# Kernel tuning notes

Hardware: AMD Instinct MI355X
Metric: run time of the kernel (lower is better)

The kernel has to match this reference:

```python
import jax, jax.numpy as jnp
import numpy as np


def _linear_interp(t, S):
    """1D linear interpolation along last axis, matching F.interpolate(mode='linear', align_corners=False).
    t: [B, C, L] -> [B, C, S]"""
    L = t.shape[-1]
    src = jnp.clip((jnp.arange(S, dtype=jnp.float32) + 0.5) * (L / S) - 0.5, 0.0, L - 1)
    i0 = jnp.floor(src).astype(jnp.int32)
    i1 = jnp.minimum(i0 + 1, L - 1)
    w = (src - i0.astype(jnp.float32)).astype(t.dtype)
    return t[..., i0] * (1.0 - w) + t[..., i1] * w


def setup_inputs() -> dict:
    key = jax.random.key(0)
    k1, k2, k3, k4 = jax.random.split(key, 4)
    B, C, H, W, L, D = 32, 768, 32, 32, 77, 512
    return {
        "img_feat": jax.random.normal(k1, (B, C, H, W), dtype=jnp.float32),
        "text_feat": jax.random.normal(k2, (B, L, D), dtype=jnp.float32),
        "W_txt": jax.random.normal(k3, (D, C), dtype=jnp.float32) / np.float32(np.sqrt(D)),
        "gamma": jax.random.normal(k4, (1,), dtype=jnp.float32) * 0.1,
    }


def reference(img_feat, text_feat, W_txt, gamma):
    B, C, H, W = img_feat.shape
    S = H * W
    q = img_feat.reshape(B, C, S)                          # [B,C,S]
    # Linear(D->C, bias=False) then transpose(1,2): [B,L,D] -> [B,C,L]
    t = jnp.einsum('bld,dc->bcl', text_feat, W_txt)
    t = _linear_interp(t, S)                               # [B,C,S]
    scale = S ** (-0.5)
    # attn = bmm(q [B,C,S], t^T [B,S,C]) * scale -> [B,C,C] channel attention
    attn = jax.nn.softmax(jnp.einsum('bis,bjs->bij', q, t) * scale, axis=-1)
    out = q + gamma * jnp.einsum('bij,bjs->bis', attn, t)  # gamma-gated residual
    return out.reshape(B, C, H, W)
```

## Files before the change

### kernel.cpp

```cpp
#include <hip/hip_runtime.h>

#define BB 32
#define CC 768
#define SS 1024
#define LLn 77
#define DD 512
#define LP 80
#define LP2 96

#define RATIO 0.0751953125f
#define IRATIO 13.298701f

#define CVT_TXT_BLOCKS (BB * LP * DD / 4 / 256)
#define CVT_W_BLOCKS ((CC / 32) * (DD / 32))
#define TG_BLOCKS (BB * 5 * 4)
#define QH_BLOCKS (256 * BB)
#define ATTN_BLOCKS (48 * BB)

typedef short bf16x8 __attribute__((ext_vector_type(8)));
typedef float f32x4 __attribute__((ext_vector_type(4)));
typedef unsigned short u16;
typedef unsigned int u32;

#define MFMA __builtin_amdgcn_mfma_f32_16x16x32_bf16

__device__ __forceinline__ u16 f2bf(float f) {
    u32 u; __builtin_memcpy(&u, &f, 4);
    u += 0x7fffu + ((u >> 16) & 1u);
    return (u16)(u >> 16);
}

__global__ __launch_bounds__(256) void k_cvt(const float* __restrict__ text,
                                             const float* __restrict__ Wt,
                                             u16* __restrict__ At,
                                             u16* __restrict__ Wb) {
    __shared__ float tile[32 * 33];
    const int bx = blockIdx.x;
    const int tid = threadIdx.x;
    if (bx < CVT_TXT_BLOCKS) {
        int j = bx * 256 + tid;
        int row80 = j >> 7, col4 = (j & 127) << 2;
        int b = row80 / LP, l = row80 - b * LP;
        u16 o[4] = {0, 0, 0, 0};
        if (l < LLn) {
            float4 v = *reinterpret_cast<const float4*>(&text[((size_t)b * LLn + l) * DD + col4]);
            o[0] = f2bf(v.x); o[1] = f2bf(v.y); o[2] = f2bf(v.z); o[3] = f2bf(v.w);
        }
        *reinterpret_cast<uint2*>(&At[(size_t)row80 * DD + col4]) = *reinterpret_cast<uint2*>(o);
    } else {
        const int bw = bx - CVT_TXT_BLOCKS;
        const int c0 = (bw % (CC / 32)) * 32, d0 = (bw / (CC / 32)) * 32;
        const int tx = tid & 31, ty = tid >> 5;
#pragma unroll
        for (int k = 0; k < 4; ++k) {
            int d = ty + k * 8;
            tile[d * 33 + tx] = Wt[(size_t)(d0 + d) * CC + c0 + tx];
        }
        __syncthreads();
#pragma unroll
        for (int k = 0; k < 4; ++k) {
            int c = ty + k * 8;
            Wb[(size_t)(c0 + c) * DD + d0 + tx] = f2bf(tile[tx * 33 + c]);
        }
    }
}

__global__ __launch_bounds__(256) void k_mid(const float* __restrict__ q,
                                             const u16* __restrict__ At,
                                             const u16* __restrict__ Wb,
                                             u16* __restrict__ qh,
                                             u16* __restrict__ tc,
                                             u16* __restrict__ tlc) {
    __shared__ float smem[3 * 1024];
    const int bx = blockIdx.x;
    const int tid = threadIdx.x;

    if (bx < TG_BLOCKS) {
        const int cg = bx / 160, mt = bx % 160;
        const int b = mt / 5, tile = mt % 5;
        const int l0 = tile * 16;
        const int w = tid >> 6, lane = tid & 63;
        const int lm = lane & 15, lg = lane >> 4;
        const int c0 = cg * 192 + w * 48;

        f32x4 acc[3];
#pragma unroll
        for (int nt = 0; nt < 3; ++nt) acc[nt] = (f32x4){0.f, 0.f, 0.f, 0.f};

        const u16* ap = At + ((size_t)b * LP + l0 + lm) * DD + lg * 8;
        const u16* bp = Wb + (size_t)(c0 + lm) * DD + lg * 8;
#pragma unroll 4
        for (int ks = 0; ks < 16; ++ks) {
            bf16x8 aq = *reinterpret_cast<const bf16x8*>(ap + ks * 32);
#pragma unroll
            for (int nt = 0; nt < 3; ++nt) {
                bf16x8 bv = *reinterpret_cast<const bf16x8*>(bp + (size_t)nt * 16 * DD + ks * 32);
                acc[nt] = MFMA(aq, bv, acc[nt], 0, 0, 0);
            }
        }

        const int lq = l0 + lg * 4;
#pragma unroll
        for (int nt = 0; nt < 3; ++nt) {
            int c = c0 + nt * 16 + lm;
            u16 pk[4];
#pragma unroll
            for (int r = 0; r < 4; ++r) pk[r] = f2bf(acc[nt][r]);
            uint2 pv; __builtin_memcpy(&pv, pk, 8);
            *reinterpret_cast<uint2*>(&tc[((size_t)b * CC + c) * LP2 + lq]) = pv;
#pragma unroll
            for (int r = 0; r < 4; ++r)
                tlc[((size_t)b * LP + lq + r) * CC + c] = pk[r];
        }
        if (tile == 4 && (tid >> 4) == (tid & 15)) { }
        if (tile == 4 && lg == 0) {
            uint4 z = {0u, 0u, 0u, 0u};
#pragma unroll
            for (int nt = 0; nt < 3; ++nt) {
                int c = c0 + nt * 16 + lm;
                *reinterpret_cast<uint4*>(&tc[((size_t)b * CC + c) * LP2 + 80]) = z;
                *reinterpret_cast<uint4*>(&tc[((size_t)b * CC + c) * LP2 + 88]) = z;
            }
        }
    } else {
        const int bxq = bx - TG_BLOCKS;
        const int b = bxq >> 8;
        const int c0 = (bxq & 255) * 3;
        for (int i4 = tid; i4 < 3 * 256; i4 += 256) {
            int r = i4 >> 8, col = (i4 & 255) << 2;
            *reinterpret_cast<float4*>(&smem[r * 1024 + col]) =
                *reinterpret_cast<const float4*>(&q[((size_t)b * CC + c0 + r) * SS + col]);
        }
        __syncthreads();
        for (int idx = tid; idx < 3 * LP2; idx += 256) {
            int r = idx / LP2, l = idx % LP2;
            float val = 0.f;
            if (l < LLn) {
                int s_lo = max(0, (int)floorf(((float)l - 0.5f) * IRATIO - 0.5f) - 1);
                int s_hi = min(SS - 1, (int)ceilf(((float)l + 1.5f) * IRATIO - 0.5f) + 1);
                float fl = (float)l;
                float a = 0.f;
                for (int s = s_lo; s <= s_hi; ++s) {
                    float src = fmaf((float)s + 0.5f, RATIO, -0.5f);
                    src = fminf(fmaxf(src, 0.f), 76.f);
                    float wgt = fmaxf(0.f, 1.f - fabsf(src - fl));
                    a = fmaf(wgt, smem[r * 1024 + s], a);
                }
                val = a * 0.03125f;
            }
            qh[((size_t)b * CC + c0 + r) * LP2 + l] = f2bf(val);
        }
    }
}

__global__ __launch_bounds__(256, 2) void k_attn_out(const u16* __restrict__ qh,
                                                     const u16* __restrict__ tc,
                                                     const u16* __restrict__ tlc,
                                                     const float* __restrict__ q,
                                                     const float* __restrict__ gamma,
                                                     float* __restrict__ out) {
    __shared__ float pmax[4][16];
    __shared__ float psum[4][16];
    __shared__ float us[16 * 80];
    __shared__ __align__(16) char pbuf[4][6400];

    const int id = blockIdx.x;
    const int o = id >> 3;
    const int b = (id & 7) * 4 + o / 48;
    const int iBase = (o % 48) * 16;
    const int tid = threadIdx.x;
    const int w = tid >> 6, lane = tid & 63;
    const int lm = lane & 15, lg = lane >> 4;
    const float g = gamma[0];

    const u16* qbase = qh + ((size_t)b * CC + iBase + lm) * LP2 + lg * 8;
    bf16x8 aq0 = *reinterpret_cast<const bf16x8*>(qbase);
    bf16x8 aq1 = *reinterpret_cast<const bf16x8*>(qbase + 32);
    bf16x8 aq2 = *reinterpret_cast<const bf16x8*>(qbase + 64);

    f32x4 acc[12];
#pragma unroll
    for (int t = 0; t < 12; ++t) acc[t] = (f32x4){0.f, 0.f, 0.f, 0.f};

    const u16* tcb = tc + ((size_t)b * CC + w * 192 + lm) * LP2 + lg * 8;
#pragma unroll
    for (int t = 0; t < 12; ++t) {
        const u16* p = tcb + (size_t)t * 16 * LP2;
        bf16x8 b0 = *reinterpret_cast<const bf16x8*>(p);
        bf16x8 b1 = *reinterpret_cast<const bf16x8*>(p + 32);
        bf16x8 b2 = *reinterpret_cast<const bf16x8*>(p + 64);
        acc[t] = MFMA(aq0, b0, acc[t], 0, 0, 0);
        acc[t] = MFMA(aq1, b1, acc[t], 0, 0, 0);
        acc[t] = MFMA(aq2, b2, acc[t], 0, 0, 0);
    }

    const size_t qBase = ((size_t)b * CC + iBase) * SS + (size_t)(tid << 2);
    f32x4 qreg[16];
#pragma unroll
    for (int r = 0; r < 16; ++r)
        qreg[r] = *reinterpret_cast<const f32x4*>(&q[qBase + (size_t)r * SS]);

    float m[4];
#pragma unroll
    for (int r = 0; r < 4; ++r) {
        float mm = acc[0][r];
#pragma unroll
        for (int t = 1; t < 12; ++t) mm = fmaxf(mm, acc[t][r]);
#pragma unroll
        for (int off = 8; off >= 1; off >>= 1) mm = fmaxf(mm, __shfl_xor(mm, off));
        m[r] = mm;
    }
    if (lm == 0) {
#pragma unroll
        for (int r = 0; r < 4; ++r) pmax[w][lg * 4 + r] = m[r];
    }
    __syncthreads();
    float gm[4];
#pragma unroll
    for (int r = 0; r < 4; ++r) {
        int row = lg * 4 + r;
        gm[r] = fmaxf(fmaxf(pmax[0][row], pmax[1][row]), fmaxf(pmax[2][row], pmax[3][row]));
    }
    float s[4] = {0.f, 0.f, 0.f, 0.f};
#pragma unroll
    for (int t = 0; t < 12; ++t) {
#pragma unroll
        for (int r = 0; r < 4; ++r) {
            float e = __expf(acc[t][r] - gm[r]);
            acc[t][r] = e;
            s[r] += e;
        }
    }
#pragma unroll
    for (int r = 0; r < 4; ++r) {
#pragma unroll
        for (int off = 8; off >= 1; off >>= 1) s[r] += __shfl_xor(s[r], off);
    }
    if (lm == 0) {
#pragma unroll
        for (int r = 0; r < 4; ++r) psum[w][lg * 4 + r] = s[r];
    }

    u16* P = (u16*)pbuf[w];
#pragma unroll
    for (int t = 0; t < 12; ++t) {
#pragma unroll
        for (int r = 0; r < 4; ++r)
            P[(lg * 4 + r) * 200 + t * 16 + lm] = f2bf(acc[t][r]);
    }

    f32x4 u[5];
#pragma unroll
    for (int nt = 0; nt < 5; ++nt) u[nt] = (f32x4){0.f, 0.f, 0.f, 0.f};
    const u16* tb = tlc + ((size_t)b * LP + lm) * CC + w * 192 + lg * 8;
#pragma unroll
    for (int ks = 0; ks < 6; ++ks) {
        bf16x8 pa = *reinterpret_cast<const bf16x8*>(&P[lm * 200 + ks * 32 + lg * 8]);
#pragma unroll
        for (int nt = 0; nt < 5; ++nt) {
            bf16x8 bv = *reinterpret_cast<const bf16x8*>(tb + (size_t)nt * 16 * CC + ks * 32);
            u[nt] = MFMA(pa, bv, u[nt], 0, 0, 0);
        }
    }

    float* up = (float*)pbuf[w];
#pragma unroll
    for (int nt = 0; nt < 5; ++nt) {
#pragma unroll
        for (int r = 0; r < 4; ++r)
            up[(lg * 4 + r) * 81 + nt * 16 + lm] = u[nt][r];
    }
    __syncthreads();
#pragma unroll
    for (int k = 0; k < 5; ++k) {
        int idx = tid + (k << 8);
        int row = idx / LP, l = idx - row * LP;
        float v = ((float*)pbuf[0])[row * 81 + l] + ((float*)pbuf[1])[row * 81 + l]
                + ((float*)pbuf[2])[row * 81 + l] + ((float*)pbuf[3])[row * 81 + l];
        float denom = psum[0][row] + psum[1][row] + psum[2][row] + psum[3][row];
        us[row * LP + l] = v / denom;
    }
    __syncthreads();

    const int s0 = tid << 2;
    float wgt[4]; int i0k[4], i1x[4];
#pragma unroll
    for (int k = 0; k < 4; ++k) {
        float src = fmaf((float)(s0 + k) + 0.5f, RATIO, -0.5f);
        src = fminf(fmaxf(src, 0.f), 76.f);
        i0k[k] = (int)src;
        wgt[k] = src - (float)i0k[k];
        i1x[k] = (i0k[k] < 76) ? i0k[k] + 1 : 76;
    }
#pragma unroll
    for (int r = 0; r < 16; ++r) {
        const float* ur = &us[r * LP];
        f32x4 ov;
#pragma unroll
        for (int k = 0; k < 4; ++k) {
            float uv = fmaf(1.f - wgt[k], ur[i0k[k]], wgt[k] * ur[i1x[k]]);
            ov[k] = qreg[r][k] + g * uv;
        }
        __builtin_nontemporal_store(ov, reinterpret_cast<f32x4*>(&out[qBase + (size_t)r * SS]));
    }
}

extern "C" void kernel_launch(void* const* d_in, const int* in_sizes, int n_in,
                              void* d_out, int out_size, void* d_ws, size_t ws_size,
                              hipStream_t stream) {
    const float* img   = (const float*)d_in[0];
    const float* text  = (const float*)d_in[1];
    const float* Wt    = (const float*)d_in[2];
    const float* gamma = (const float*)d_in[3];
    float* out = (float*)d_out;
    char* ws = (char*)d_ws;
    u16*   tc_bf  = (u16*)(ws);
    u16*   tlc_bf = (u16*)(ws + 4718592);
    u16*   qh_bf  = (u16*)(ws + 8650752);
    u16*   At_bf  = (u16*)(ws + 13369344);
    u16*   Wb_bf  = (u16*)(ws + 15990784);

    k_cvt<<<dim3(CVT_TXT_BLOCKS + CVT_W_BLOCKS), 256, 0, stream>>>(text, Wt, At_bf, Wb_bf);
    k_mid<<<dim3(TG_BLOCKS + QH_BLOCKS), 256, 0, stream>>>(img, At_bf, Wb_bf, qh_bf, tc_bf, tlc_bf);
    k_attn_out<<<dim3(ATTN_BLOCKS), 256, 0, stream>>>(qh_bf, tc_bf, tlc_bf, img, gamma, out);
}
```

Baseline: 98.28 us.

## Precompute interpolation-transpose weights and read q windows directly without LDS

The qh projection (q times the transposed interpolation matrix) no longer stages three full 1024-float rows in shared memory and recomputes the interpolation weights per element. A small 96x36 weight table is now built once in the conversion kernel. Each thread then loads a 36-float aligned window of q straight from global memory and does a dot product with the table row. This removes the full-row LDS staging and barrier and most of the per-tap ALU work, at the cost of overlapping global reads across neighbouring threads and an extra workspace buffer.

```diff
diff --git a/kernel.cpp b/kernel.cpp
--- a/kernel.cpp
+++ b/kernel.cpp
@@ -13,6 +13,7 @@
 
 #define CVT_TXT_BLOCKS (BB * LP * DD / 4 / 256)
 #define CVT_W_BLOCKS ((CC / 32) * (DD / 32))
+#define WT_BLOCKS 14
 #define TG_BLOCKS (BB * 5 * 4)
 #define QH_BLOCKS (256 * BB)
 #define ATTN_BLOCKS (48 * BB)
@@ -30,10 +31,17 @@
     return (u16)(u >> 16);
 }
 
+__device__ __forceinline__ int win_base(int l) {
+    int s_lo = max(0, (int)floorf(((float)l - 0.5f) * IRATIO - 0.5f) - 1);
+    int base = s_lo & ~3;
+    return min(base, SS - 36);
+}
+
 __global__ __launch_bounds__(256) void k_cvt(const float* __restrict__ text,
                                              const float* __restrict__ Wt,
                                              u16* __restrict__ At,
-                                             u16* __restrict__ Wb) {
+                                             u16* __restrict__ Wb,
+                                             float* __restrict__ wtab_g) {
     __shared__ float tile[32 * 33];
     const int bx = blockIdx.x;
     const int tid = threadIdx.x;
@@ -47,7 +55,7 @@
             o[0] = f2bf(v.x); o[1] = f2bf(v.y); o[2] = f2bf(v.z); o[3] = f2bf(v.w);
         }
         *reinterpret_cast<uint2*>(&At[(size_t)row80 * DD + col4]) = *reinterpret_cast<uint2*>(o);
-    } else {
+    } else if (bx < CVT_TXT_BLOCKS + CVT_W_BLOCKS) {
         const int bw = bx - CVT_TXT_BLOCKS;
         const int c0 = (bw % (CC / 32)) * 32, d0 = (bw / (CC / 32)) * 32;
         const int tx = tid & 31, ty = tid >> 5;
@@ -62,16 +70,29 @@
             int c = ty + k * 8;
             Wb[(size_t)(c0 + c) * DD + d0 + tx] = f2bf(tile[tx * 33 + c]);
         }
+    } else {
+        int idx = (bx - CVT_TXT_BLOCKS - CVT_W_BLOCKS) * 256 + tid;
+        if (idx < 96 * 36) {
+            int l = idx / 36, j = idx - l * 36;
+            float wgt = 0.f;
+            if (l < LLn) {
+                int s = win_base(l) + j;
+                float src = fmaf((float)s + 0.5f, RATIO, -0.5f);
+                src = fminf(fmaxf(src, 0.f), 76.f);
+                wgt = fmaxf(0.f, 1.f - fabsf(src - (float)l));
+            }
+            wtab_g[l * 36 + j] = wgt;
+        }
     }
 }
 
 __global__ __launch_bounds__(256) void k_mid(const float* __restrict__ q,
                                              const u16* __restrict__ At,
                                              const u16* __restrict__ Wb,
+                                             const float* __restrict__ wtab_g,
                                              u16* __restrict__ qh,
                                              u16* __restrict__ tc,
                                              u16* __restrict__ tlc) {
-    __shared__ float smem[3 * 1024];
     const int bx = blockIdx.x;
     const int tid = threadIdx.x;
 
@@ -112,7 +133,6 @@
             for (int r = 0; r < 4; ++r)
                 tlc[((size_t)b * LP + lq + r) * CC + c] = pk[r];
         }
-        if (tile == 4 && (tid >> 4) == (tid & 15)) { }
         if (tile == 4 && lg == 0) {
             uint4 z = {0u, 0u, 0u, 0u};
 #pragma unroll
@@ -126,29 +146,30 @@
         const int bxq = bx - TG_BLOCKS;
         const int b = bxq >> 8;
         const int c0 = (bxq & 255) * 3;
-        for (int i4 = tid; i4 < 3 * 256; i4 += 256) {
-            int r = i4 >> 8, col = (i4 & 255) << 2;
-            *reinterpret_cast<float4*>(&smem[r * 1024 + col]) =
-                *reinterpret_cast<const float4*>(&q[((size_t)b * CC + c0 + r) * SS + col]);
-        }
-        __syncthreads();
-        for (int idx = tid; idx < 3 * LP2; idx += 256) {
-            int r = idx / LP2, l = idx % LP2;
-            float val = 0.f;
+#pragma unroll
+        for (int k = 0; k < 2; ++k) {
+            int idx = tid + (k << 8);
+            if (idx >= 3 * LP2) break;
+            int r = idx / LP2, l = idx - r * LP2;
+            u16 o = 0;
             if (l < LLn) {
-                int s_lo = max(0, (int)floorf(((float)l - 0.5f) * IRATIO - 0.5f) - 1);
-                int s_hi = min(SS - 1, (int)ceilf(((float)l + 1.5f) * IRATIO - 0.5f) + 1);
-                float fl = (float)l;
+                const int base = win_base(l);
+                const f32x4* qp = reinterpret_cast<const f32x4*>(
+                    &q[((size_t)b * CC + c0 + r) * SS + base]);
+                const f32x4* wp = reinterpret_cast<const f32x4*>(&wtab_g[l * 36]);
+                f32x4 qv[9], wv[9];
+#pragma unroll
+                for (int j = 0; j < 9; ++j) { qv[j] = qp[j]; wv[j] = wp[j]; }
                 float a = 0.f;
-                for (int s = s_lo; s <= s_hi; ++s) {
-                    float src = fmaf((float)s + 0.5f, RATIO, -0.5f);
-                    src = fminf(fmaxf(src, 0.f), 76.f);
-                    float wgt = fmaxf(0.f, 1.f - fabsf(src - fl));
-                    a = fmaf(wgt, smem[r * 1024 + s], a);
+#pragma unroll
+                for (int j = 0; j < 9; ++j) {
+#pragma unroll
+                    for (int e = 0; e < 4; ++e)
+                        a = fmaf(qv[j][e], wv[j][e], a);
                 }
-                val = a * 0.03125f;
+                o = f2bf(a * 0.03125f);
             }
-            qh[((size_t)b * CC + c0 + r) * LP2 + l] = f2bf(val);
+            qh[((size_t)b * CC + c0 + r) * LP2 + l] = o;
         }
     }
 }
@@ -319,8 +340,11 @@
     u16*   qh_bf  = (u16*)(ws + 8650752);
     u16*   At_bf  = (u16*)(ws + 13369344);
     u16*   Wb_bf  = (u16*)(ws + 15990784);
-
-    k_cvt<<<dim3(CVT_TXT_BLOCKS + CVT_W_BLOCKS), 256, 0, stream>>>(text, Wt, At_bf, Wb_bf);
-    k_mid<<<dim3(TG_BLOCKS + QH_BLOCKS), 256, 0, stream>>>(img, At_bf, Wb_bf, qh_bf, tc_bf, tlc_bf);
+    float* wtab_g = (float*)(ws + 16777216);
+
+    k_cvt<<<dim3(CVT_TXT_BLOCKS + CVT_W_BLOCKS + WT_BLOCKS), 256, 0, stream>>>(
+        text, Wt, At_bf, Wb_bf, wtab_g);
+    k_mid<<<dim3(TG_BLOCKS + QH_BLOCKS), 256, 0, stream>>>(
+        img, At_bf, Wb_bf, wtab_g, qh_bf, tc_bf, tlc_bf);
     k_attn_out<<<dim3(ATTN_BLOCKS), 256, 0, stream>>>(qh_bf, tc_bf, tlc_bf, img, gamma, out);
 }
```

After: 108.2 us. 1.1x slower.
